# Kernel tuning notes

Measured on AMD Instinct MI355X. Metric: run time of the kernel, lower is better.

## Reference

```python
import jax, jax.numpy as jnp
import numpy as np

DIM = 256          # model dim
HK = 8             # kv heads
HQ = 32            # query heads
H = HQ // HK       # queries per kv group
DH = 128           # head dim (== DIM//2, required by RoPE assert)
B = 1
T = 2048
THETA = 10000.0
CACHE = 8192       # RoPE cached seq_len; module uses _freqs_cis[-T:]


def _rope(x):
    # x: [..., T, DH]; positions are the LAST T of the cached 8192 (faithful to _freqs_cis[-T:])
    t = x.shape[-2]
    half = DH  # == DIM // 2
    pos = jnp.arange(CACHE - t, CACHE, dtype=jnp.float32)
    inv_freq = THETA ** (-(jnp.arange(half, dtype=jnp.float32) / half))
    f = pos[:, None] * inv_freq[None, :]            # [T, DH]
    cos, sin = jnp.cos(f), jnp.sin(f)
    x1, x2 = jnp.split(x, 2, axis=-1)
    rot = jnp.concatenate((-x2, x1), axis=-1)       # rotate_half
    return x * cos + rot * sin


def setup_inputs() -> dict:
    key = jax.random.key(0)
    ks = jax.random.split(key, 7)
    q = jax.random.normal(ks[0], (B, T, DIM), jnp.float32)
    k = jax.random.normal(ks[1], (B, T, DIM), jnp.float32)
    v = jax.random.normal(ks[2], (B, T, DIM), jnp.float32)
    mask = jnp.tril(jnp.ones((T, T), dtype=bool))   # causal
    Wq = jax.random.normal(ks[3], (DIM, HQ * DH), jnp.float32) * 0.02
    Wk = jax.random.normal(ks[4], (DIM, HK * DH), jnp.float32) * 0.02
    Wv = jax.random.normal(ks[5], (DIM, HK * DH), jnp.float32) * 0.02
    Wo = jax.random.normal(ks[6], (HQ * DH, DIM), jnp.float32) * 0.02
    return {"q": q, "k": k, "v": v, "mask": mask, "Wq": Wq, "Wk": Wk, "Wv": Wv, "Wo": Wo}


def reference(q, k, v, mask, Wq, Wk, Wv, Wo):
    b, t, _ = q.shape
    # projections + head split; query heads grouped as (HK, H)
    qi = (q @ Wq).reshape(b, t, HQ, DH).transpose(0, 2, 1, 3).reshape(b, HK, H, t, DH)
    ki = (k @ Wk).reshape(b, t, HK, DH).transpose(0, 2, 1, 3)  # [b, HK, t, DH]
    vi = (v @ Wv).reshape(b, t, HK, DH).transpose(0, 2, 1, 3)  # [b, HK, t, DH]
    # RoPE on q, k AND v (module applies _apply_rope to all three)
    qi = _rope(qi)
    ki = _rope(ki)
    vi = _rope(vi)
    s = jnp.einsum('bghid,bgjd->bghij', qi, ki) / jnp.sqrt(jnp.asarray(DH, qi.dtype))
    neg = -jnp.finfo(s.dtype).max
    s = jnp.where(mask, s, neg)
    attn = jax.nn.softmax(s, axis=-1)               # [b, HK, H, t, t]
    vals = jnp.einsum('bghij,bgjd->bghid', attn, vi)
    vals = vals.transpose(0, 3, 1, 2, 4).reshape(b, t, HQ * DH)
    return vals @ Wo
```

## Files before the change

kernel.cpp:

```cpp
#include <hip/hip_runtime.h>
#include <hip/hip_bf16.h>
#include <math.h>

#define TSEQ 2048
#define NHQ 32
#define NHK 8
#define DH 128

typedef __attribute__((ext_vector_type(8))) short short8;
typedef __attribute__((ext_vector_type(4))) float f32x4;
typedef __attribute__((ext_vector_type(4))) short s16x4;

__device__ __forceinline__ short f2bf(float f) {
  union { float f; unsigned u; } v; v.f = f;
  unsigned r = v.u + 0x7fffu + ((v.u >> 16) & 1u);
  return (short)(r >> 16);
}

__device__ __forceinline__ f32x4 zero4() {
  f32x4 z; z[0] = 0.f; z[1] = 0.f; z[2] = 0.f; z[3] = 0.f; return z;
}

__device__ __forceinline__ void async_cp16(const short* g, short* l) {
  __builtin_amdgcn_global_load_lds(
      (const __attribute__((address_space(1))) unsigned int*)g,
      (__attribute__((address_space(3))) unsigned int*)l, 16, 0, 0);
}

__global__ __launch_bounds__(256) void prep_transpose_kernel(
    const float* __restrict__ q, const float* __restrict__ k,
    const float* __restrict__ v, short* __restrict__ qkv,
    float* __restrict__ cosT, float* __restrict__ sinT,
    const float* __restrict__ Wq, const float* __restrict__ Wk,
    const float* __restrict__ Wv, const float* __restrict__ Wo,
    short* __restrict__ WqT, short* __restrict__ WkT,
    short* __restrict__ WvT, short* __restrict__ WoT) {
  __shared__ short tl[64][65];
  int bx = blockIdx.x, tid = threadIdx.x;
  if (bx < 1792) {
    int gid = bx * 256 + tid;
    if (gid < 393216) {
      int i4 = gid * 4;
      const float* src = (i4 < 524288) ? (q + i4)
                       : (i4 < 1048576 ? (k + i4 - 524288) : (v + i4 - 1048576));
      float f0 = src[0], f1 = src[1], f2 = src[2], f3 = src[3];
      s16x4 o; o[0] = f2bf(f0); o[1] = f2bf(f1); o[2] = f2bf(f2); o[3] = f2bf(f3);
      *(s16x4*)&qkv[i4] = o;
    } else if (gid < 458752) {
      int idx = (gid - 393216) * 4;
      int t = idx >> 7, d0 = idx & 127;
      float pos = (float)(8192 - TSEQ + t);
#pragma unroll
      for (int jj = 0; jj < 4; ++jj) {
        int d = d0 + jj;
        float inv = exp2f(-0.10381025296522977f * (float)d);
        float f = pos * inv;
        cosT[t * 128 + d] = cosf(f);
        sinT[t * 128 + d] = sinf(f);
      }
    }
    return;
  }
  int b = bx - 1792;
  const float* S; short* D; int K, N, tr, tc;
  if (b < 256)      { S = Wq; D = WqT; K = 256;  N = 4096; tr = b >> 6;        tc = b & 63; }
  else if (b < 320) { S = Wk; D = WkT; K = 256;  N = 1024; int t = b - 256; tr = t >> 4; tc = t & 15; }
  else if (b < 384) { S = Wv; D = WvT; K = 256;  N = 1024; int t = b - 320; tr = t >> 4; tc = t & 15; }
  else              { S = Wo; D = WoT; K = 4096; N = 256;  int t = b - 384; tr = t >> 2; tc = t & 3; }
  int k0 = tr * 64, n0 = tc * 64;
#pragma unroll
  for (int it = 0; it < 4; ++it) {
    int r = it * 16 + (tid >> 4), c = (tid & 15) * 4;
    const float* s = &S[(size_t)(k0 + r) * N + n0 + c];
    tl[r][c + 0] = f2bf(s[0]); tl[r][c + 1] = f2bf(s[1]);
    tl[r][c + 2] = f2bf(s[2]); tl[r][c + 3] = f2bf(s[3]);
  }
  __syncthreads();
#pragma unroll
  for (int it = 0; it < 4; ++it) {
    int rr = it * 16 + (tid >> 4), cc = (tid & 15) * 4;
    s16x4 o;
    o[0] = tl[cc + 0][rr]; o[1] = tl[cc + 1][rr];
    o[2] = tl[cc + 2][rr]; o[3] = tl[cc + 3][rr];
    *(s16x4*)&D[(size_t)(n0 + rr) * K + k0 + cc] = o;
  }
}

#define SCALE 0.08838834764831845f

__global__ __launch_bounds__(256) void proj_kernel(
    const short* __restrict__ qkv,
    const short* __restrict__ WqT, const short* __restrict__ WkT,
    const short* __restrict__ WvT,
    const float* __restrict__ cosT, const float* __restrict__ sinT,
    short* __restrict__ Qr, short* __restrict__ Kr, short* __restrict__ Vt) {
  __shared__ short As[64 * 64];
  __shared__ short Bs[128 * 64];
  int tid = threadIdx.x, lane = tid & 63, w = tid >> 6;
  int i = lane & 15, grp = lane >> 4;
  int bh = blockIdx.y, r0 = blockIdx.x * 64;
  const short* X; const short* Wt; short* dst; int vmode = 0;
  float oscale = 1.0f;
  if (bh < 32)      { X = qkv;                Wt = WqT + bh * (128 * 256);        dst = Qr + (size_t)bh * TSEQ * DH; oscale = SCALE; }
  else if (bh < 40) { X = qkv + TSEQ * 256;   Wt = WkT + (bh - 32) * (128 * 256); dst = Kr + (size_t)(bh - 32) * TSEQ * DH; }
  else              { X = qkv + 2 * TSEQ * 256; Wt = WvT + (bh - 40) * (128 * 256); dst = Vt + (size_t)(bh - 40) * DH * TSEQ; vmode = 1; }

  f32x4 acc[8];
#pragma unroll
  for (int n = 0; n < 8; ++n) acc[n] = zero4();

  for (int kc = 0; kc < 4; ++kc) {
    __syncthreads();
    {
      int row = tid >> 2, p = tid & 3;
      const short* src = X + (size_t)(r0 + row) * 256 + kc * 64 + p * 16;
      short8 d0 = *(const short8*)(src);
      short8 d1 = *(const short8*)(src + 8);
      int c0 = p * 2;
      *(short8*)&As[row * 64 + ((c0 ^ (row & 7)) * 8)] = d0;
      *(short8*)&As[row * 64 + (((c0 + 1) ^ (row & 7)) * 8)] = d1;
    }
    {
      int row = tid >> 1, p = tid & 1;
      const short* src = Wt + (size_t)row * 256 + kc * 64 + p * 32;
#pragma unroll
      for (int jj = 0; jj < 4; ++jj) {
        short8 dv = *(const short8*)(src + jj * 8);
        int c0 = p * 4 + jj;
        *(short8*)&Bs[row * 64 + ((c0 ^ (row & 7)) * 8)] = dv;
      }
    }
    __syncthreads();
#pragma unroll
    for (int kc2 = 0; kc2 < 2; ++kc2) {
      short8 a = *(const short8*)&As[(w * 16 + i) * 64 + (((kc2 * 4 + grp) ^ (i & 7)) * 8)];
#pragma unroll
      for (int n = 0; n < 8; ++n) {
        short8 bf = *(const short8*)&Bs[(n * 16 + i) * 64 + (((kc2 * 4 + grp) ^ (i & 7)) * 8)];
        acc[n] = __builtin_amdgcn_mfma_f32_16x16x32_bf16(a, bf, acc[n], 0, 0, 0);
      }
    }
  }
#pragma unroll
  for (int r = 0; r < 4; ++r) {
    int t = r0 + w * 16 + grp * 4 + r;
    const float* cr = cosT + (size_t)t * 128;
    const float* sr = sinT + (size_t)t * 128;
#pragma unroll
    for (int n = 0; n < 8; ++n) {
      int d = n * 16 + i;
      float x = acc[n][r];
      float xp = acc[n ^ 4][r];
      float rot = (n < 4) ? -xp : xp;
      float val = (x * cr[d] + rot * sr[d]) * oscale;
      short bv = f2bf(val);
      if (vmode) dst[(size_t)d * TSEQ + t] = bv;
      else       dst[(size_t)t * DH + d] = bv;
    }
  }
}

__global__ __launch_bounds__(512, 2) void attn_kernel(
    const short* __restrict__ Qr, const short* __restrict__ Kr,
    const short* __restrict__ Vt, short* __restrict__ Oa) {
  __shared__ __attribute__((aligned(16))) short Ks[2][64 * 128];
  __shared__ __attribute__((aligned(16))) short Vs[2][128 * 64];
  __shared__ short Ps[8][16 * 72];
  int tid = threadIdx.x, lane = tid & 63, w = tid >> 6;
  int i = lane & 15, grp = lane >> 4;
  int b = blockIdx.x;
  int hk = b & 7, hq = (b >> 3) & 3, pr = b >> 5;
  int h = hk * 4 + hq;
  const short* Qh = Qr + (size_t)h * TSEQ * DH;
  const short* Kh = Kr + (size_t)hk * TSEQ * DH;
  const short* Vh = Vt + (size_t)hk * DH * TSEQ;

  for (int half = 0; half < 2; ++half) {
    int qt = half ? pr : (15 - pr);
    int q0 = qt * 128;
    int qrow = q0 + w * 16 + i;
    short8 qf[4];
#pragma unroll
    for (int c = 0; c < 4; ++c)
      qf[c] = *(const short8*)&Qh[(size_t)qrow * DH + c * 32 + grp * 8];

    f32x4 oacc[8];
#pragma unroll
    for (int n = 0; n < 8; ++n) oacc[n] = zero4();
    float mrow[4], lsum[4];
#pragma unroll
    for (int r = 0; r < 4; ++r) { mrow[r] = -3.0e38f; lsum[r] = 0.0f; }

    int nt = 2 * qt + 2;
    int wave_max_row = q0 + w * 16 + 15;

    auto stage = [&](int kt_, int bsel) {
      int kv0_ = kt_ * 64;
#pragma unroll
      for (int hf = 0; hf < 2; ++hf) {
        int ci = hf * 512 + w * 64 + lane;
        int row = ci >> 4, c = ci & 15;
        async_cp16(Kh + (size_t)(kv0_ + row) * DH + ((c ^ (row & 15)) << 3),
                   &Ks[bsel][hf * 4096 + w * 512]);
      }
#pragma unroll
      for (int hf = 0; hf < 2; ++hf) {
        int ci = hf * 512 + w * 64 + lane;
        int row = ci >> 3, c = ci & 7;
        async_cp16(Vh + (size_t)row * TSEQ + kv0_ + ((c ^ (row & 7)) << 3),
                   &Vs[bsel][hf * 4096 + w * 512]);
      }
    };

    stage(0, 0);
    for (int kt = 0; kt < nt; ++kt) {
      int kv0 = kt * 64;
      int buf = kt & 1;
      if (kt + 1 < nt) {
        stage(kt + 1, buf ^ 1);
        asm volatile("s_waitcnt vmcnt(4)" ::: "memory");
      } else {
        asm volatile("s_waitcnt vmcnt(0)" ::: "memory");
      }
      __builtin_amdgcn_s_barrier();
      if (kv0 <= wave_max_row) {
        const short* Kb = &Ks[buf][0];
        const short* Vb = &Vs[buf][0];
        f32x4 sacc[4];
#pragma unroll
        for (int n = 0; n < 4; ++n) sacc[n] = zero4();
        __builtin_amdgcn_s_setprio(1);
#pragma unroll
        for (int c = 0; c < 4; ++c) {
#pragma unroll
          for (int n = 0; n < 4; ++n) {
            short8 kb = *(const short8*)&Kb[(n * 16 + i) * 128 + (((c * 4 + grp) ^ i) * 8)];
            sacc[n] = __builtin_amdgcn_mfma_f32_16x16x32_bf16(qf[c], kb, sacc[n], 0, 0, 0);
          }
        }
        __builtin_amdgcn_s_setprio(0);
        bool diag = (kt >= nt - 2);
        float p_[4][4];
#pragma unroll
        for (int n = 0; n < 4; ++n)
#pragma unroll
          for (int r = 0; r < 4; ++r) {
            float s = sacc[n][r];
            if (diag) {
              int qq = q0 + w * 16 + grp * 4 + r;
              int kk = kv0 + n * 16 + i;
              if (kk > qq) s = -3.0e38f;
            }
            p_[n][r] = s;
          }
        float mnew[4];
#pragma unroll
        for (int r = 0; r < 4; ++r)
          mnew[r] = fmaxf(fmaxf(p_[0][r], p_[1][r]), fmaxf(p_[2][r], p_[3][r]));
#pragma unroll
        for (int off = 1; off <= 8; off <<= 1)
#pragma unroll
          for (int r = 0; r < 4; ++r)
            mnew[r] = fmaxf(mnew[r], __shfl_xor(mnew[r], off));
        bool ok = true;
#pragma unroll
        for (int r = 0; r < 4; ++r) ok = ok && (mnew[r] <= mrow[r] + 8.0f);
        if (!__all(ok ? 1 : 0)) {
#pragma unroll
          for (int r = 0; r < 4; ++r) {
            float mn = fmaxf(mrow[r], mnew[r]);
            float sfv = __expf(mrow[r] - mn);
            mrow[r] = mn;
            lsum[r] *= sfv;
#pragma unroll
            for (int n = 0; n < 8; ++n) oacc[n][r] *= sfv;
          }
        }
#pragma unroll
        for (int n = 0; n < 4; ++n)
#pragma unroll
          for (int r = 0; r < 4; ++r) {
            float p = __expf(p_[n][r] - mrow[r]);
            lsum[r] += p;
            Ps[w][(grp * 4 + r) * 72 + n * 16 + i] = f2bf(p);
          }
        __builtin_amdgcn_s_setprio(1);
#pragma unroll
        for (int kc = 0; kc < 2; ++kc) {
          short8 pa = *(const short8*)&Ps[w][i * 72 + kc * 32 + grp * 8];
#pragma unroll
          for (int n = 0; n < 8; ++n) {
            short8 vb = *(const short8*)&Vb[(n * 16 + i) * 64 + (((kc * 4 + grp) ^ (i & 7)) * 8)];
            oacc[n] = __builtin_amdgcn_mfma_f32_16x16x32_bf16(pa, vb, oacc[n], 0, 0, 0);
          }
        }
        __builtin_amdgcn_s_setprio(0);
      }
      __builtin_amdgcn_s_barrier();
    }
#pragma unroll
    for (int off = 1; off <= 8; off <<= 1)
#pragma unroll
      for (int r = 0; r < 4; ++r) lsum[r] += __shfl_xor(lsum[r], off);
#pragma unroll
    for (int r = 0; r < 4; ++r) {
      int t = q0 + w * 16 + grp * 4 + r;
      float inv = 1.0f / lsum[r];
#pragma unroll
      for (int n = 0; n < 8; ++n) {
        int d = n * 16 + i;
        Oa[(size_t)t * 4096 + h * 128 + d] = f2bf(oacc[n][r] * inv);
      }
    }
  }
}

__global__ __launch_bounds__(256) void outproj_kernel(
    const short* __restrict__ Oa, const short* __restrict__ WoT,
    float* __restrict__ Opart) {
  __shared__ short As[128 * 64];
  __shared__ short Bs[64 * 64];
  int tid = threadIdx.x, lane = tid & 63, w = tid >> 6;
  int i = lane & 15, grp = lane >> 4;
  int m0 = blockIdx.x * 128, n0 = blockIdx.y * 64, z = blockIdx.z;
  f32x4 acc[2][4];
#pragma unroll
  for (int mf = 0; mf < 2; ++mf)
#pragma unroll
    for (int nf = 0; nf < 4; ++nf) acc[mf][nf] = zero4();
  for (int kc = z * 16; kc < z * 16 + 16; ++kc) {
    __syncthreads();
    {
      int row = tid >> 1, p = tid & 1;
      const short* src = Oa + (size_t)(m0 + row) * 4096 + kc * 64 + p * 32;
#pragma unroll
      for (int jj = 0; jj < 4; ++jj) {
        short8 dv = *(const short8*)(src + jj * 8);
        int c0 = p * 4 + jj;
        *(short8*)&As[row * 64 + ((c0 ^ (row & 7)) * 8)] = dv;
      }
    }
    {
      int row = tid >> 2, p = tid & 3;
      const short* src = WoT + (size_t)(n0 + row) * 4096 + kc * 64 + p * 16;
      short8 d0 = *(const short8*)src;
      short8 d1 = *(const short8*)(src + 8);
      int c0 = p * 2;
      *(short8*)&Bs[row * 64 + ((c0 ^ (row & 7)) * 8)] = d0;
      *(short8*)&Bs[row * 64 + (((c0 + 1) ^ (row & 7)) * 8)] = d1;
    }
    __syncthreads();
#pragma unroll
    for (int kc2 = 0; kc2 < 2; ++kc2) {
#pragma unroll
      for (int mf = 0; mf < 2; ++mf) {
        short8 a = *(const short8*)&As[(w * 32 + mf * 16 + i) * 64 + (((kc2 * 4 + grp) ^ (i & 7)) * 8)];
#pragma unroll
        for (int nf = 0; nf < 4; ++nf) {
          short8 b = *(const short8*)&Bs[(nf * 16 + i) * 64 + (((kc2 * 4 + grp) ^ (i & 7)) * 8)];
          acc[mf][nf] = __builtin_amdgcn_mfma_f32_16x16x32_bf16(a, b, acc[mf][nf], 0, 0, 0);
        }
      }
    }
  }
  float* dst = Opart + (size_t)z * (TSEQ * 256);
#pragma unroll
  for (int mf = 0; mf < 2; ++mf)
#pragma unroll
    for (int r = 0; r < 4; ++r) {
      int t = m0 + w * 32 + mf * 16 + grp * 4 + r;
#pragma unroll
      for (int nf = 0; nf < 4; ++nf)
        dst[(size_t)t * 256 + n0 + nf * 16 + i] = acc[mf][nf][r];
    }
}

__global__ __launch_bounds__(256) void reduce_kernel(
    const float* __restrict__ Opart, float* __restrict__ out) {
  int gid = blockIdx.x * 256 + threadIdx.x;
  int i4 = gid * 4;
  f32x4 s = *(const f32x4*)&Opart[i4];
#pragma unroll
  for (int z = 1; z < 4; ++z) {
    f32x4 p = *(const f32x4*)&Opart[(size_t)z * (TSEQ * 256) + i4];
    s[0] += p[0]; s[1] += p[1]; s[2] += p[2]; s[3] += p[3];
  }
  *(f32x4*)&out[i4] = s;
}

extern "C" void kernel_launch(void* const* d_in, const int* in_sizes, int n_in,
                              void* d_out, int out_size, void* d_ws, size_t ws_size,
                              hipStream_t stream) {
  const float* q  = (const float*)d_in[0];
  const float* k  = (const float*)d_in[1];
  const float* v  = (const float*)d_in[2];
  const float* Wq = (const float*)d_in[4];
  const float* Wk = (const float*)d_in[5];
  const float* Wv = (const float*)d_in[6];
  const float* Wo = (const float*)d_in[7];
  float* out = (float*)d_out;

  char* p = (char*)d_ws;
  auto take = [&](size_t nbytes) {
    char* r = p; p += (nbytes + 255) & ~(size_t)255; return r;
  };
  short* qkv  = (short*)take(3ull * TSEQ * 256 * 2);
  short* WqT  = (short*)take(4096ull * 256 * 2);
  short* WkT  = (short*)take(1024ull * 256 * 2);
  short* WvT  = (short*)take(1024ull * 256 * 2);
  short* WoT  = (short*)take(256ull * 4096 * 2);
  float* cosT = (float*)take((size_t)TSEQ * 128 * 4);
  float* sinT = (float*)take((size_t)TSEQ * 128 * 4);
  short* Qr   = (short*)take((size_t)NHQ * TSEQ * DH * 2);
  short* Kr   = (short*)take((size_t)NHK * TSEQ * DH * 2);
  short* Vt   = (short*)take((size_t)NHK * TSEQ * DH * 2);
  short* Oa   = (short*)take((size_t)TSEQ * 4096 * 2);
  float* Opart = (float*)Qr;

  hipLaunchKernelGGL(prep_transpose_kernel, dim3(2432), dim3(256), 0, stream,
                     q, k, v, qkv, cosT, sinT,
                     Wq, Wk, Wv, Wo, WqT, WkT, WvT, WoT);
  hipLaunchKernelGGL(proj_kernel, dim3(32, 48), dim3(256), 0, stream,
                     qkv, WqT, WkT, WvT, cosT, sinT, Qr, Kr, Vt);
  hipLaunchKernelGGL(attn_kernel, dim3(256), dim3(512), 0, stream,
                     Qr, Kr, Vt, Oa);
  hipLaunchKernelGGL(outproj_kernel, dim3(16, 4, 4), dim3(256), 0, stream,
                     Oa, WoT, Opart);
  hipLaunchKernelGGL(reduce_kernel, dim3(512), dim3(256), 0, stream,
                     Opart, out);
}
```

Baseline: 228.2 us.

## Double-buffer projection GEMMs with async LDS loads and transpose attention score layout

The projection and output-projection GEMMs now stage tiles through double-buffered shared memory using async global-to-LDS copies with precomputed swizzled source pointers, so the next K chunk loads while the current one computes. In attention, the QK^T MFMA operands are swapped so each lane holds a single query row. That shrinks the online-softmax max and sum reductions to two cross-group shuffles and uses packed bf16 conversion for the P tile stores. K/V staging address arithmetic is hoisted out of the loop. The rescale condition changes from all-lanes-ok to any-lane-exceeds, and the extra barriers and doubled LDS could lower occupancy.

```diff
diff --git a/kernel.cpp b/kernel.cpp
--- a/kernel.cpp
+++ b/kernel.cpp
@@ -94,8 +94,8 @@
     const short* __restrict__ WvT,
     const float* __restrict__ cosT, const float* __restrict__ sinT,
     short* __restrict__ Qr, short* __restrict__ Kr, short* __restrict__ Vt) {
-  __shared__ short As[64 * 64];
-  __shared__ short Bs[128 * 64];
+  __shared__ __attribute__((aligned(16))) short As[2][64 * 64];
+  __shared__ __attribute__((aligned(16))) short Bs[2][128 * 64];
   int tid = threadIdx.x, lane = tid & 63, w = tid >> 6;
   int i = lane & 15, grp = lane >> 4;
   int bh = blockIdx.y, r0 = blockIdx.x * 64;
@@ -105,41 +105,53 @@
   else if (bh < 40) { X = qkv + TSEQ * 256;   Wt = WkT + (bh - 32) * (128 * 256); dst = Kr + (size_t)(bh - 32) * TSEQ * DH; }
   else              { X = qkv + 2 * TSEQ * 256; Wt = WvT + (bh - 40) * (128 * 256); dst = Vt + (size_t)(bh - 40) * DH * TSEQ; vmode = 1; }
 
+  const short* srcA[2];
+#pragma unroll
+  for (int j = 0; j < 2; ++j) {
+    int ci = w * 128 + j * 64 + lane;
+    int row = ci >> 3, c = ci & 7;
+    srcA[j] = X + (size_t)(r0 + row) * 256 + ((c ^ (row & 7)) << 3);
+  }
+  const short* srcB[4];
+#pragma unroll
+  for (int j = 0; j < 4; ++j) {
+    int ci = w * 256 + j * 64 + lane;
+    int row = ci >> 3, c = ci & 7;
+    srcB[j] = Wt + (size_t)row * 256 + ((c ^ (row & 7)) << 3);
+  }
+  auto stage = [&](int kc_, int bsel) {
+#pragma unroll
+    for (int j = 0; j < 2; ++j)
+      async_cp16(srcA[j] + kc_ * 64, &As[bsel][(w * 128 + j * 64) * 8]);
+#pragma unroll
+    for (int j = 0; j < 4; ++j)
+      async_cp16(srcB[j] + kc_ * 64, &Bs[bsel][(w * 256 + j * 64) * 8]);
+  };
+
   f32x4 acc[8];
 #pragma unroll
   for (int n = 0; n < 8; ++n) acc[n] = zero4();
 
+  stage(0, 0);
   for (int kc = 0; kc < 4; ++kc) {
-    __syncthreads();
-    {
-      int row = tid >> 2, p = tid & 3;
-      const short* src = X + (size_t)(r0 + row) * 256 + kc * 64 + p * 16;
-      short8 d0 = *(const short8*)(src);
-      short8 d1 = *(const short8*)(src + 8);
-      int c0 = p * 2;
-      *(short8*)&As[row * 64 + ((c0 ^ (row & 7)) * 8)] = d0;
-      *(short8*)&As[row * 64 + (((c0 + 1) ^ (row & 7)) * 8)] = d1;
-    }
-    {
-      int row = tid >> 1, p = tid & 1;
-      const short* src = Wt + (size_t)row * 256 + kc * 64 + p * 32;
-#pragma unroll
-      for (int jj = 0; jj < 4; ++jj) {
-        short8 dv = *(const short8*)(src + jj * 8);
-        int c0 = p * 4 + jj;
-        *(short8*)&Bs[row * 64 + ((c0 ^ (row & 7)) * 8)] = dv;
-      }
-    }
-    __syncthreads();
+    int buf = kc & 1;
+    if (kc < 3) {
+      stage(kc + 1, buf ^ 1);
+      asm volatile("s_waitcnt vmcnt(6)" ::: "memory");
+    } else {
+      asm volatile("s_waitcnt vmcnt(0)" ::: "memory");
+    }
+    __builtin_amdgcn_s_barrier();
 #pragma unroll
     for (int kc2 = 0; kc2 < 2; ++kc2) {
-      short8 a = *(const short8*)&As[(w * 16 + i) * 64 + (((kc2 * 4 + grp) ^ (i & 7)) * 8)];
+      short8 a = *(const short8*)&As[buf][(w * 16 + i) * 64 + (((kc2 * 4 + grp) ^ (i & 7)) * 8)];
 #pragma unroll
       for (int n = 0; n < 8; ++n) {
-        short8 bf = *(const short8*)&Bs[(n * 16 + i) * 64 + (((kc2 * 4 + grp) ^ (i & 7)) * 8)];
+        short8 bf = *(const short8*)&Bs[buf][(n * 16 + i) * 64 + (((kc2 * 4 + grp) ^ (i & 7)) * 8)];
         acc[n] = __builtin_amdgcn_mfma_f32_16x16x32_bf16(a, bf, acc[n], 0, 0, 0);
       }
     }
+    __builtin_amdgcn_s_barrier();
   }
 #pragma unroll
   for (int r = 0; r < 4; ++r) {
@@ -165,7 +177,7 @@
     const short* __restrict__ Vt, short* __restrict__ Oa) {
   __shared__ __attribute__((aligned(16))) short Ks[2][64 * 128];
   __shared__ __attribute__((aligned(16))) short Vs[2][128 * 64];
-  __shared__ short Ps[8][16 * 72];
+  __shared__ __attribute__((aligned(16))) short Ps[8][16 * 72];
   int tid = threadIdx.x, lane = tid & 63, w = tid >> 6;
   int i = lane & 15, grp = lane >> 4;
   int b = blockIdx.x;
@@ -175,41 +187,39 @@
   const short* Kh = Kr + (size_t)hk * TSEQ * DH;
   const short* Vh = Vt + (size_t)hk * DH * TSEQ;
 
+  const short* kst[2]; const short* vst[2];
+#pragma unroll
+  for (int hf = 0; hf < 2; ++hf) {
+    int ci = hf * 512 + w * 64 + lane;
+    int rk = ci >> 4, ck = ci & 15;
+    kst[hf] = Kh + (size_t)rk * DH + ((ck ^ (rk & 15)) << 3);
+    int rv = ci >> 3, cv = ci & 7;
+    vst[hf] = Vh + (size_t)rv * TSEQ + ((cv ^ (rv & 7)) << 3);
+  }
+
   for (int half = 0; half < 2; ++half) {
     int qt = half ? pr : (15 - pr);
     int q0 = qt * 128;
-    int qrow = q0 + w * 16 + i;
+    int qq = q0 + w * 16 + i;
     short8 qf[4];
 #pragma unroll
     for (int c = 0; c < 4; ++c)
-      qf[c] = *(const short8*)&Qh[(size_t)qrow * DH + c * 32 + grp * 8];
+      qf[c] = *(const short8*)&Qh[(size_t)qq * DH + c * 32 + grp * 8];
 
     f32x4 oacc[8];
 #pragma unroll
     for (int n = 0; n < 8; ++n) oacc[n] = zero4();
-    float mrow[4], lsum[4];
-#pragma unroll
-    for (int r = 0; r < 4; ++r) { mrow[r] = -3.0e38f; lsum[r] = 0.0f; }
+    float mrow = -3.0e38f, lsum = 0.0f;
 
     int nt = 2 * qt + 2;
     int wave_max_row = q0 + w * 16 + 15;
 
     auto stage = [&](int kt_, int bsel) {
       int kv0_ = kt_ * 64;
-#pragma unroll
-      for (int hf = 0; hf < 2; ++hf) {
-        int ci = hf * 512 + w * 64 + lane;
-        int row = ci >> 4, c = ci & 15;
-        async_cp16(Kh + (size_t)(kv0_ + row) * DH + ((c ^ (row & 15)) << 3),
-                   &Ks[bsel][hf * 4096 + w * 512]);
-      }
-#pragma unroll
-      for (int hf = 0; hf < 2; ++hf) {
-        int ci = hf * 512 + w * 64 + lane;
-        int row = ci >> 3, c = ci & 7;
-        async_cp16(Vh + (size_t)row * TSEQ + kv0_ + ((c ^ (row & 7)) << 3),
-                   &Vs[bsel][hf * 4096 + w * 512]);
-      }
+      async_cp16(kst[0] + (size_t)kv0_ * DH, &Ks[bsel][w * 512]);
+      async_cp16(kst[1] + (size_t)kv0_ * DH, &Ks[bsel][4096 + w * 512]);
+      async_cp16(vst[0] + kv0_, &Vs[bsel][w * 512]);
+      async_cp16(vst[1] + kv0_, &Vs[bsel][4096 + w * 512]);
     };
 
     stage(0, 0);
@@ -235,7 +245,7 @@
 #pragma unroll
           for (int n = 0; n < 4; ++n) {
             short8 kb = *(const short8*)&Kb[(n * 16 + i) * 128 + (((c * 4 + grp) ^ i) * 8)];
-            sacc[n] = __builtin_amdgcn_mfma_f32_16x16x32_bf16(qf[c], kb, sacc[n], 0, 0, 0);
+            sacc[n] = __builtin_amdgcn_mfma_f32_16x16x32_bf16(kb, qf[c], sacc[n], 0, 0, 0);
           }
         }
         __builtin_amdgcn_s_setprio(0);
@@ -247,43 +257,46 @@
           for (int r = 0; r < 4; ++r) {
             float s = sacc[n][r];
             if (diag) {
-              int qq = q0 + w * 16 + grp * 4 + r;
-              int kk = kv0 + n * 16 + i;
+              int kk = kv0 + n * 16 + grp * 4 + r;
               if (kk > qq) s = -3.0e38f;
             }
             p_[n][r] = s;
           }
-        float mnew[4];
-#pragma unroll
-        for (int r = 0; r < 4; ++r)
-          mnew[r] = fmaxf(fmaxf(p_[0][r], p_[1][r]), fmaxf(p_[2][r], p_[3][r]));
-#pragma unroll
-        for (int off = 1; off <= 8; off <<= 1)
-#pragma unroll
-          for (int r = 0; r < 4; ++r)
-            mnew[r] = fmaxf(mnew[r], __shfl_xor(mnew[r], off));
-        bool ok = true;
-#pragma unroll
-        for (int r = 0; r < 4; ++r) ok = ok && (mnew[r] <= mrow[r] + 8.0f);
-        if (!__all(ok ? 1 : 0)) {
-#pragma unroll
-          for (int r = 0; r < 4; ++r) {
-            float mn = fmaxf(mrow[r], mnew[r]);
-            float sfv = __expf(mrow[r] - mn);
-            mrow[r] = mn;
-            lsum[r] *= sfv;
-#pragma unroll
-            for (int n = 0; n < 8; ++n) oacc[n][r] *= sfv;
+        float mnew = p_[0][0];
+#pragma unroll
+        for (int n = 0; n < 4; ++n)
+#pragma unroll
+          for (int r = 0; r < 4; ++r) mnew = fmaxf(mnew, p_[n][r]);
+        mnew = fmaxf(mnew, __shfl_xor(mnew, 16));
+        mnew = fmaxf(mnew, __shfl_xor(mnew, 32));
+        if (__any((mnew > mrow + 8.0f) ? 1 : 0)) {
+          float mn = fmaxf(mrow, mnew);
+          float sfv = __expf(mrow - mn);
+          mrow = mn;
+          lsum *= sfv;
+          float sf0 = __shfl(sfv, grp * 4 + 0);
+          float sf1 = __shfl(sfv, grp * 4 + 1);
+          float sf2 = __shfl(sfv, grp * 4 + 2);
+          float sf3 = __shfl(sfv, grp * 4 + 3);
+#pragma unroll
+          for (int n = 0; n < 8; ++n) {
+            oacc[n][0] *= sf0; oacc[n][1] *= sf1;
+            oacc[n][2] *= sf2; oacc[n][3] *= sf3;
           }
         }
 #pragma unroll
-        for (int n = 0; n < 4; ++n)
-#pragma unroll
-          for (int r = 0; r < 4; ++r) {
-            float p = __expf(p_[n][r] - mrow[r]);
-            lsum[r] += p;
-            Ps[w][(grp * 4 + r) * 72 + n * 16 + i] = f2bf(p);
-          }
+        for (int n = 0; n < 4; ++n) {
+          float e0 = __expf(p_[n][0] - mrow);
+          float e1 = __expf(p_[n][1] - mrow);
+          float e2 = __expf(p_[n][2] - mrow);
+          float e3 = __expf(p_[n][3] - mrow);
+          lsum += (e0 + e1) + (e2 + e3);
+          unsigned lo, hi;
+          asm("v_cvt_pk_bf16_f32 %0, %1, %2" : "=v"(lo) : "v"(e0), "v"(e1));
+          asm("v_cvt_pk_bf16_f32 %0, %1, %2" : "=v"(hi) : "v"(e2), "v"(e3));
+          *(unsigned long long*)&Ps[w][i * 72 + n * 16 + grp * 4] =
+              ((unsigned long long)hi << 32) | lo;
+        }
         __builtin_amdgcn_s_setprio(1);
 #pragma unroll
         for (int kc = 0; kc < 2; ++kc) {
@@ -298,18 +311,18 @@
       }
       __builtin_amdgcn_s_barrier();
     }
-#pragma unroll
-    for (int off = 1; off <= 8; off <<= 1)
-#pragma unroll
-      for (int r = 0; r < 4; ++r) lsum[r] += __shfl_xor(lsum[r], off);
+    lsum += __shfl_xor(lsum, 16);
+    lsum += __shfl_xor(lsum, 32);
+    float inv[4];
+#pragma unroll
+    for (int r = 0; r < 4; ++r) inv[r] = 1.0f / __shfl(lsum, grp * 4 + r);
 #pragma unroll
     for (int r = 0; r < 4; ++r) {
       int t = q0 + w * 16 + grp * 4 + r;
-      float inv = 1.0f / lsum[r];
 #pragma unroll
       for (int n = 0; n < 8; ++n) {
         int d = n * 16 + i;
-        Oa[(size_t)t * 4096 + h * 128 + d] = f2bf(oacc[n][r] * inv);
+        Oa[(size_t)t * 4096 + h * 128 + d] = f2bf(oacc[n][r] * inv[r]);
       }
     }
   }
@@ -318,50 +331,64 @@
 __global__ __launch_bounds__(256) void outproj_kernel(
     const short* __restrict__ Oa, const short* __restrict__ WoT,
     float* __restrict__ Opart) {
-  __shared__ short As[128 * 64];
-  __shared__ short Bs[64 * 64];
+  __shared__ __attribute__((aligned(16))) short As[2][128 * 64];
+  __shared__ __attribute__((aligned(16))) short Bs[2][64 * 64];
   int tid = threadIdx.x, lane = tid & 63, w = tid >> 6;
   int i = lane & 15, grp = lane >> 4;
   int m0 = blockIdx.x * 128, n0 = blockIdx.y * 64, z = blockIdx.z;
+
+  const short* srcA[4];
+#pragma unroll
+  for (int j = 0; j < 4; ++j) {
+    int ci = w * 256 + j * 64 + lane;
+    int row = ci >> 3, c = ci & 7;
+    srcA[j] = Oa + (size_t)(m0 + row) * 4096 + (size_t)z * 1024 + ((c ^ (row & 7)) << 3);
+  }
+  const short* srcB[2];
+#pragma unroll
+  for (int j = 0; j < 2; ++j) {
+    int ci = w * 128 + j * 64 + lane;
+    int row = ci >> 3, c = ci & 7;
+    srcB[j] = WoT + (size_t)(n0 + row) * 4096 + (size_t)z * 1024 + ((c ^ (row & 7)) << 3);
+  }
+  auto stage = [&](int kc_, int bsel) {
+#pragma unroll
+    for (int j = 0; j < 4; ++j)
+      async_cp16(srcA[j] + kc_ * 64, &As[bsel][(w * 256 + j * 64) * 8]);
+#pragma unroll
+    for (int j = 0; j < 2; ++j)
+      async_cp16(srcB[j] + kc_ * 64, &Bs[bsel][(w * 128 + j * 64) * 8]);
+  };
+
   f32x4 acc[2][4];
 #pragma unroll
   for (int mf = 0; mf < 2; ++mf)
 #pragma unroll
     for (int nf = 0; nf < 4; ++nf) acc[mf][nf] = zero4();
-  for (int kc = z * 16; kc < z * 16 + 16; ++kc) {
-    __syncthreads();
-    {
-      int row = tid >> 1, p = tid & 1;
-      const short* src = Oa + (size_t)(m0 + row) * 4096 + kc * 64 + p * 32;
-#pragma unroll
-      for (int jj = 0; jj < 4; ++jj) {
-        short8 dv = *(const short8*)(src + jj * 8);
-        int c0 = p * 4 + jj;
-        *(short8*)&As[row * 64 + ((c0 ^ (row & 7)) * 8)] = dv;
-      }
-    }
-    {
-      int row = tid >> 2, p = tid & 3;
-      const short* src = WoT + (size_t)(n0 + row) * 4096 + kc * 64 + p * 16;
-      short8 d0 = *(const short8*)src;
-      short8 d1 = *(const short8*)(src + 8);
-      int c0 = p * 2;
-      *(short8*)&Bs[row * 64 + ((c0 ^ (row & 7)) * 8)] = d0;
-      *(short8*)&Bs[row * 64 + (((c0 + 1) ^ (row & 7)) * 8)] = d1;
-    }
-    __syncthreads();
+
+  stage(0, 0);
+  for (int kc = 0; kc < 16; ++kc) {
+    int buf = kc & 1;
+    if (kc < 15) {
+      stage(kc + 1, buf ^ 1);
+      asm volatile("s_waitcnt vmcnt(6)" ::: "memory");
+    } else {
+      asm volatile("s_waitcnt vmcnt(0)" ::: "memory");
+    }
+    __builtin_amdgcn_s_barrier();
 #pragma unroll
     for (int kc2 = 0; kc2 < 2; ++kc2) {
 #pragma unroll
       for (int mf = 0; mf < 2; ++mf) {
-        short8 a = *(const short8*)&As[(w * 32 + mf * 16 + i) * 64 + (((kc2 * 4 + grp) ^ (i & 7)) * 8)];
+        short8 a = *(const short8*)&As[buf][(w * 32 + mf * 16 + i) * 64 + (((kc2 * 4 + grp) ^ (i & 7)) * 8)];
 #pragma unroll
         for (int nf = 0; nf < 4; ++nf) {
-          short8 b = *(const short8*)&Bs[(nf * 16 + i) * 64 + (((kc2 * 4 + grp) ^ (i & 7)) * 8)];
-          acc[mf][nf] = __builtin_amdgcn_mfma_f32_16x16x32_bf16(a, b, acc[mf][nf], 0, 0, 0);
+          short8 bb = *(const short8*)&Bs[buf][(nf * 16 + i) * 64 + (((kc2 * 4 + grp) ^ (i & 7)) * 8)];
+          acc[mf][nf] = __builtin_amdgcn_mfma_f32_16x16x32_bf16(a, bb, acc[mf][nf], 0, 0, 0);
         }
       }
     }
+    __builtin_amdgcn_s_barrier();
   }
   float* dst = Opart + (size_t)z * (TSEQ * 256);
 #pragma unroll
```

Measured after the change: 200.3 us. 12.2% less time.
